# Optimization experiments

Hardware: AMD Instinct MI355X
Metric: run time of the kernel (lower is better)

## Reference

```python
import jax, jax.numpy as jnp
import numpy as np

H = 4          # number of GCN heads (hard-coded self.h = 4)
EPS = 1e-6     # MWPToolkit LayerNorm eps
B, K, D, HID = 16, 1024, 256, 256
DK = D // H


def setup_inputs() -> dict:
    key = jax.random.key(0)
    ks = jax.random.split(key, 12)
    sc = lambda fan_in: 1.0 / np.sqrt(fan_in).astype(np.float32)
    return {
        "graph_nodes": jax.random.normal(ks[0], (B, K, D), jnp.float32),
        "graph": jax.random.randint(ks[1], (B, 5, K, K), 0, 2, jnp.int32),
        # per-head GCN layer 1: GraphConvolution(indim -> hiddim)
        "Wg1": jax.random.normal(ks[2], (H, D, HID), jnp.float32) * sc(D),
        "bg1": jax.random.normal(ks[3], (H, HID), jnp.float32) * sc(D),
        # per-head GCN layer 2: GraphConvolution(hiddim -> d_k)
        "Wg2": jax.random.normal(ks[4], (H, HID, DK), jnp.float32) * sc(HID),
        "bg2": jax.random.normal(ks[5], (H, DK), jnp.float32) * sc(HID),
        # PositionwiseFeedForward: Linear(indim,hiddim) -> ReLU -> Linear(hiddim,outdim)
        "Wf1": jax.random.normal(ks[6], (D, HID), jnp.float32) * sc(D),
        "bf1": jax.random.normal(ks[7], (HID,), jnp.float32) * sc(D),
        "Wf2": jax.random.normal(ks[8], (HID, D), jnp.float32) * sc(HID),
        "bf2": jax.random.normal(ks[9], (D,), jnp.float32) * sc(HID),
        # LayerNorm(outdim) affine params
        "ln_a": jnp.ones((D,), jnp.float32),
        "ln_b": jnp.zeros((D,), jnp.float32),
    }


def reference(graph_nodes, graph, Wg1, bg1, Wg2, bg2, Wf1, bf1, Wf2, bf2, ln_a, ln_b):
    adj = graph.astype(jnp.float32)                      # (B, 5, K, K)
    # adj_list = [adj[:,1], adj[:,1], adj[:,4], adj[:,4]] -> stack heads
    adj_h = jnp.stack([adj[:, 1], adj[:, 1], adj[:, 4], adj[:, 4]])  # (H,B,K,K)

    # GCN layer 1 (all heads at once): relu(adj @ (x @ W1) + b1)
    sup1 = jnp.einsum('bkd,hdf->hbkf', graph_nodes, Wg1)            # (H,B,K,HID)
    h1 = jax.nn.relu(jnp.einsum('hbkj,hbjf->hbkf', adj_h, sup1)
                     + bg1[:, None, None, :])
    # (dropout is identity in eval)
    # GCN layer 2: adj @ (h1 @ W2) + b2
    sup2 = jnp.einsum('hbkf,hfe->hbke', h1, Wg2)                    # (H,B,K,DK)
    h2 = jnp.einsum('hbkj,hbje->hbke', adj_h, sup2) + bg2[:, None, None, :]

    # concat heads along feature dim: (B,K,H*DK) == (B,K,D)
    g = jnp.transpose(h2, (1, 2, 0, 3)).reshape(h2.shape[1], h2.shape[2], -1)

    # MWPToolkit LayerNorm: a*(x-mean)/(std+eps)+b, std unbiased (ddof=1)
    mu = g.mean(-1, keepdims=True)
    sd = jnp.std(g, axis=-1, keepdims=True, ddof=1)
    g = ln_a * (g - mu) / (sd + EPS) + ln_b + graph_nodes           # residual

    # PositionwiseFeedForward + residual (dropout identity in eval)
    ff = jax.nn.relu(g @ Wf1 + bf1) @ Wf2 + bf2
    out = ff + g
    return adj, out
```

## Files before the change

### kernel.cpp

```cpp
#include <hip/hip_runtime.h>

typedef unsigned short ushort_t;
using short8  = __attribute__((ext_vector_type(8))) short;
using floatx4 = __attribute__((ext_vector_type(4))) float;

__device__ __forceinline__ ushort_t f2bf(float f) {
  unsigned int x = __builtin_bit_cast(unsigned int, f);
  x += 0x7fffu + ((x >> 16) & 1u);
  return (ushort_t)(x >> 16);
}

__device__ __forceinline__ void gld16(const ushort_t* g, ushort_t* l) {
  __builtin_amdgcn_global_load_lds(
      (const __attribute__((address_space(1))) void*)(unsigned long long)(uintptr_t)g,
      (__attribute__((address_space(3))) void*)l, 16, 0, 0);
}

template <typename F>
__device__ __forceinline__ void gemm_tile(const ushort_t* __restrict__ A, int lda,
                                          const ushort_t* __restrict__ BT, int ldb,
                                          int K, F epi) {
  __shared__ ushort_t As[128 * 32];
  __shared__ ushort_t Bs[128 * 32];

  const int tid  = threadIdx.x;
  const int wave = tid >> 6;
  const int lane = tid & 63;
  const int l15  = lane & 15;
  const int quad = lane >> 4;
  const int wm   = wave >> 1;
  const int wn   = wave & 1;

  const int srow   = lane >> 2;
  const int schunk = (lane & 3) ^ ((lane >> 3) & 3);
  const int scol   = schunk * 8;

  const ushort_t* gA0 = A  + (size_t)(wave * 32 + srow) * lda + scol;
  const ushort_t* gA1 = gA0 + (size_t)16 * lda;
  const ushort_t* gB0 = BT + (size_t)(wave * 32 + srow) * ldb + scol;
  const ushort_t* gB1 = gB0 + (size_t)16 * ldb;
  ushort_t* lA0 = As + (wave * 32) * 32;
  ushort_t* lA1 = As + (wave * 32 + 16) * 32;
  ushort_t* lB0 = Bs + (wave * 32) * 32;
  ushort_t* lB1 = Bs + (wave * 32 + 16) * 32;

  floatx4 acc[4][4] = {};

  const int chunk_sw = quad ^ ((l15 >> 1) & 3);
  const int aoff = (wm * 64 + l15) * 32 + chunk_sw * 8;
  const int boff = (wn * 64 + l15) * 32 + chunk_sw * 8;

  for (int k0 = 0; k0 < K; k0 += 32) {
    gld16(gA0, lA0); gld16(gA1, lA1);
    gld16(gB0, lB0); gld16(gB1, lB1);
    gA0 += 32; gA1 += 32; gB0 += 32; gB1 += 32;
    __syncthreads();
    short8 af[4], bfr[4];
#pragma unroll
    for (int i = 0; i < 4; i++) af[i]  = *(const short8*)(As + aoff + i * 512);
#pragma unroll
    for (int j = 0; j < 4; j++) bfr[j] = *(const short8*)(Bs + boff + j * 512);
#pragma unroll
    for (int i = 0; i < 4; i++)
#pragma unroll
      for (int j = 0; j < 4; j++)
        acc[i][j] = __builtin_amdgcn_mfma_f32_16x16x32_bf16(af[i], bfr[j], acc[i][j], 0, 0, 0);
    __syncthreads();
  }

#pragma unroll
  for (int i = 0; i < 4; i++)
#pragma unroll
    for (int j = 0; j < 4; j++)
#pragma unroll
      for (int r = 0; r < 4; r++)
        epi(wm * 64 + i * 16 + quad * 4 + r, wn * 64 + j * 16 + l15, acc[i][j][r]);
}


__global__ __launch_bounds__(256) void k_cast(const int* __restrict__ graph,
                                              float* __restrict__ adj_out,
                                              ushort_t* __restrict__ adjb) {
  const size_t i = (size_t)blockIdx.x * 256 + threadIdx.x;
  int4 v = ((const int4*)graph)[i];
  float4 f = make_float4((float)v.x, (float)v.y, (float)v.z, (float)v.w);
  ((float4*)adj_out)[i] = f;
  const size_t e0 = i * 4;
  const unsigned sb = (unsigned)(e0 >> 20);
  const unsigned s = sb % 5u, b = sb / 5u;
  if (s == 1u || s == 4u) {
    const unsigned tt = (s == 4u) ? 1u : 0u;
    ushort4 h;
    h.x = f2bf(f.x); h.y = f2bf(f.y); h.z = f2bf(f.z); h.w = f2bf(f.w);
    *(ushort4*)(adjb + (((size_t)(b * 2 + tt)) << 20) + (e0 & 0xFFFFFu)) = h;
  }
}

__global__ __launch_bounds__(256) void k_castX(const float* __restrict__ gn,
                                               ushort_t* __restrict__ Xb) {
  const size_t i = (size_t)blockIdx.x * 256 + threadIdx.x;
  float4 f = ((const float4*)gn)[i];
  ushort4 h; h.x = f2bf(f.x); h.y = f2bf(f.y); h.z = f2bf(f.z); h.w = f2bf(f.w);
  ((ushort4*)Xb)[i] = h;
}

__global__ __launch_bounds__(256) void k_prepw(const float* __restrict__ Wg1, const float* __restrict__ Wg2,
                                               const float* __restrict__ Wf1, const float* __restrict__ Wf2,
                                               ushort_t* __restrict__ W1T, ushort_t* __restrict__ Wg2bd,
                                               ushort_t* __restrict__ Wf1T, ushort_t* __restrict__ Wf2T) {
  const int i = blockIdx.x * 256 + threadIdx.x;
  if (i < 262144) {
    const int fI = i >> 8, d = i & 255;
    const int h = fI >> 8, ff = fI & 255;
    W1T[i] = f2bf(Wg1[((h << 8) + d) * 256 + ff]);
  } else if (i < 524288) {
    const int j = i - 262144;
    const int r = j >> 10, c = j & 1023;
    const int h = r >> 6, e = r & 63;
    const float v = ((c >> 8) == h) ? Wg2[((h << 8) + (c & 255)) * 64 + e] : 0.f;
    Wg2bd[j] = f2bf(v);
  } else if (i < 589824) {
    const int j = i - 524288;
    const int n = j >> 8, k = j & 255;
    Wf1T[j] = f2bf(Wf1[k * 256 + n]);
  } else if (i < 655360) {
    const int j = i - 589824;
    const int n = j >> 8, k = j & 255;
    Wf2T[j] = f2bf(Wf2[k * 256 + n]);
  }
}


__global__ __launch_bounds__(256) void k_g1(const ushort_t* __restrict__ W1T,
                                            const ushort_t* __restrict__ Xb,
                                            ushort_t* __restrict__ sup1T) {
  const int nt = blockIdx.x, mt = blockIdx.y, b = blockIdx.z;
  const ushort_t* A  = W1T + (size_t)mt * 128 * 256;
  const ushort_t* BT = Xb + (size_t)b * 262144 + (size_t)nt * 128 * 256;
  ushort_t* C = sup1T + ((size_t)b << 20);
  gemm_tile(A, 256, BT, 256, 256, [&](int r, int c, float v) {
    C[(size_t)(mt * 128 + r) * 1024 + nt * 128 + c] = f2bf(v);
  });
}

__global__ __launch_bounds__(256) void k_g2(const ushort_t* __restrict__ adjb,
                                            const ushort_t* __restrict__ sup1T,
                                            const float* __restrict__ bg1,
                                            ushort_t* __restrict__ h1) {
  const int nt = blockIdx.x, mt = blockIdx.y, b = blockIdx.z;
  const int t = nt >> 2;
  const ushort_t* A  = adjb + ((size_t)(b * 2 + t) << 20) + (size_t)mt * 128 * 1024;
  const ushort_t* BT = sup1T + ((size_t)b << 20) + (size_t)nt * 128 * 1024;
  ushort_t* C = h1 + ((size_t)b << 20);
  const float* bias = bg1 + nt * 128;
  gemm_tile(A, 1024, BT, 1024, 1024, [&](int r, int c, float v) {
    C[(size_t)(mt * 128 + r) * 1024 + nt * 128 + c] = f2bf(fmaxf(v + bias[c], 0.f));
  });
}

__global__ __launch_bounds__(256) void k_g3(const ushort_t* __restrict__ Wg2bd,
                                            const ushort_t* __restrict__ h1,
                                            ushort_t* __restrict__ sup2T) {
  const int nt = blockIdx.x, mt = blockIdx.y, b = blockIdx.z;
  const ushort_t* A  = Wg2bd + (size_t)mt * 128 * 1024;
  const ushort_t* BT = h1 + ((size_t)b << 20) + (size_t)nt * 128 * 1024;
  ushort_t* C = sup2T + (size_t)b * 262144;
  gemm_tile(A, 1024, BT, 1024, 1024, [&](int r, int c, float v) {
    C[(size_t)(mt * 128 + r) * 1024 + nt * 128 + c] = f2bf(v);
  });
}

__global__ __launch_bounds__(256) void k_g4(const ushort_t* __restrict__ adjb,
                                            const ushort_t* __restrict__ sup2T,
                                            const float* __restrict__ bg2,
                                            float* __restrict__ g) {
  const int nt = blockIdx.x, mt = blockIdx.y, b = blockIdx.z;
  const ushort_t* A  = adjb + ((size_t)(b * 2 + nt) << 20) + (size_t)mt * 128 * 1024;
  const ushort_t* BT = sup2T + (size_t)b * 262144 + (size_t)nt * 128 * 1024;
  float* C = g + (size_t)b * 262144;
  const float* bias = bg2 + nt * 128;
  gemm_tile(A, 1024, BT, 1024, 1024, [&](int r, int c, float v) {
    C[(size_t)(mt * 128 + r) * 256 + nt * 128 + c] = v + bias[c];
  });
}

__global__ __launch_bounds__(256) void k_ln(const float* __restrict__ g, const float* __restrict__ gn,
                                            const float* __restrict__ la, const float* __restrict__ lb,
                                            float* __restrict__ glnf, ushort_t* __restrict__ glnb) {
  const int row = blockIdx.x * 4 + (threadIdx.x >> 6);
  const int lane = threadIdx.x & 63;
  const float4 x = ((const float4*)(g + (size_t)row * 256))[lane];
  float s = x.x + x.y + x.z + x.w;
#pragma unroll
  for (int o = 1; o < 64; o <<= 1) s += __shfl_xor(s, o);
  const float mu = s * (1.f / 256.f);
  const float dx = x.x - mu, dy = x.y - mu, dz = x.z - mu, dw = x.w - mu;
  float q = dx * dx + dy * dy + dz * dz + dw * dw;
#pragma unroll
  for (int o = 1; o < 64; o <<= 1) q += __shfl_xor(q, o);
  const float inv = 1.f / (sqrtf(q * (1.f / 255.f)) + 1e-6f);
  const float4 a  = ((const float4*)la)[lane];
  const float4 bb = ((const float4*)lb)[lane];
  const float4 rz = ((const float4*)(gn + (size_t)row * 256))[lane];
  float4 o;
  o.x = a.x * dx * inv + bb.x + rz.x;
  o.y = a.y * dy * inv + bb.y + rz.y;
  o.z = a.z * dz * inv + bb.z + rz.z;
  o.w = a.w * dw * inv + bb.w + rz.w;
  ((float4*)(glnf + (size_t)row * 256))[lane] = o;
  ushort4 h; h.x = f2bf(o.x); h.y = f2bf(o.y); h.z = f2bf(o.z); h.w = f2bf(o.w);
  ((ushort4*)(glnb + (size_t)row * 256))[lane] = h;
}

__global__ __launch_bounds__(256) void k_f1(const ushort_t* __restrict__ gln,
                                            const ushort_t* __restrict__ Wf1T,
                                            const float* __restrict__ bf1,
                                            ushort_t* __restrict__ tb) {
  const int nt = blockIdx.x, mt = blockIdx.y;
  const ushort_t* A  = gln + (size_t)mt * 128 * 256;
  const ushort_t* BT = Wf1T + (size_t)nt * 128 * 256;
  const float* bias = bf1 + nt * 128;
  gemm_tile(A, 256, BT, 256, 256, [&](int r, int c, float v) {
    tb[(size_t)(mt * 128 + r) * 256 + nt * 128 + c] = f2bf(fmaxf(v + bias[c], 0.f));
  });
}

__global__ __launch_bounds__(256) void k_f2(const ushort_t* __restrict__ tb,
                                            const ushort_t* __restrict__ Wf2T,
                                            const float* __restrict__ bf2,
                                            const float* __restrict__ glnf,
                                            float* __restrict__ out) {
  const int nt = blockIdx.x, mt = blockIdx.y;
  const ushort_t* A  = tb + (size_t)mt * 128 * 256;
  const ushort_t* BT = Wf2T + (size_t)nt * 128 * 256;
  const float* bias = bf2 + nt * 128;
  gemm_tile(A, 256, BT, 256, 256, [&](int r, int c, float v) {
    const size_t idx = (size_t)(mt * 128 + r) * 256 + nt * 128 + c;
    out[idx] = v + bias[c] + glnf[idx];
  });
}

extern "C" void kernel_launch(void* const* d_in, const int* in_sizes, int n_in,
                              void* d_out, int out_size, void* d_ws, size_t ws_size,
                              hipStream_t stream) {
  const float* gnodes = (const float*)d_in[0];
  const int*   graph  = (const int*)d_in[1];
  const float* Wg1 = (const float*)d_in[2];
  const float* bg1 = (const float*)d_in[3];
  const float* Wg2 = (const float*)d_in[4];
  const float* bg2 = (const float*)d_in[5];
  const float* Wf1 = (const float*)d_in[6];
  const float* bf1 = (const float*)d_in[7];
  const float* Wf2 = (const float*)d_in[8];
  const float* bf2 = (const float*)d_in[9];
  const float* ln_a = (const float*)d_in[10];
  const float* ln_b = (const float*)d_in[11];

  float* adj_out = (float*)d_out;
  float* out     = (float*)d_out + 83886080;

  char* ws = (char*)d_ws;
  ushort_t* adjb  = (ushort_t*)(ws);
  ushort_t* Xb    = (ushort_t*)(ws + 67108864);
  ushort_t* W1T   = (ushort_t*)(ws + 75497472);
  ushort_t* Wg2bd = (ushort_t*)(ws + 76021760);
  ushort_t* Wf1T  = (ushort_t*)(ws + 76546048);
  ushort_t* Wf2T  = (ushort_t*)(ws + 76677120);
  ushort_t* sup1T = (ushort_t*)(ws + 76808192);
  ushort_t* h1    = (ushort_t*)(ws + 110362624);
  ushort_t* sup2T = (ushort_t*)(ws + 143917056);
  float*    gbuf  = (float*)(ws + 76808192);
  float*    glnf  = (float*)(ws + 76808192 + 16777216);
  ushort_t* glnb  = (ushort_t*)(ws + 110362624);
  ushort_t* tbuf  = (ushort_t*)(ws + 110362624 + 8388608);

  k_cast <<<81920, 256, 0, stream>>>(graph, adj_out, adjb);
  k_castX<<<4096, 256, 0, stream>>>(gnodes, Xb);
  k_prepw<<<2560, 256, 0, stream>>>(Wg1, Wg2, Wf1, Wf2, W1T, Wg2bd, Wf1T, Wf2T);

  k_g1<<<dim3(8, 8, 16), 256, 0, stream>>>(W1T, Xb, sup1T);
  k_g2<<<dim3(8, 8, 16), 256, 0, stream>>>(adjb, sup1T, bg1, h1);
  k_g3<<<dim3(8, 2, 16), 256, 0, stream>>>(Wg2bd, h1, sup2T);
  k_g4<<<dim3(2, 8, 16), 256, 0, stream>>>(adjb, sup2T, bg2, gbuf);

  k_ln<<<4096, 256, 0, stream>>>(gbuf, gnodes, ln_a, ln_b, glnf, glnb);

  k_f1<<<dim3(2, 128), 256, 0, stream>>>(glnb, Wf1T, bf1, tbuf);
  k_f2<<<dim3(2, 128), 256, 0, stream>>>(tbuf, Wf2T, bf2, glnf, out);
}
```

Baseline: 736.4 us.

## Reassociate first GCN layer as (adj@X)@W1 and deepen GEMM K-tile to 64

Layer 1 now computes adj@X once per adjacency type (two per batch), then multiplies by the per-head W1. The previous code did adj@(X@W1) across all four heads with an inner dimension of 1024, so this cuts the large adjacency GEMM work roughly in half. It adds a transposed bf16 copy of X and splits the adjacency cast so the f32 adj output is written by its own kernel at the end. The shared GEMM tile also loads 64 K-elements per stage with a new swizzle, halving the number of barriers per tile. This uses more LDS per block, and the extra bf16 rounding of AX changes numerics slightly.

```diff
diff --git a/kernel.cpp b/kernel.cpp
--- a/kernel.cpp
+++ b/kernel.cpp
@@ -20,8 +20,8 @@
 __device__ __forceinline__ void gemm_tile(const ushort_t* __restrict__ A, int lda,
                                           const ushort_t* __restrict__ BT, int ldb,
                                           int K, F epi) {
-  __shared__ ushort_t As[128 * 32];
-  __shared__ ushort_t Bs[128 * 32];
+  __shared__ ushort_t As[128 * 64];
+  __shared__ ushort_t Bs[128 * 64];
 
   const int tid  = threadIdx.x;
   const int wave = tid >> 6;
@@ -31,40 +31,43 @@
   const int wm   = wave >> 1;
   const int wn   = wave & 1;
 
-  const int srow   = lane >> 2;
-  const int schunk = (lane & 3) ^ ((lane >> 3) & 3);
-  const int scol   = schunk * 8;
-
-  const ushort_t* gA0 = A  + (size_t)(wave * 32 + srow) * lda + scol;
-  const ushort_t* gA1 = gA0 + (size_t)16 * lda;
-  const ushort_t* gB0 = BT + (size_t)(wave * 32 + srow) * ldb + scol;
-  const ushort_t* gB1 = gB0 + (size_t)16 * ldb;
-  ushort_t* lA0 = As + (wave * 32) * 32;
-  ushort_t* lA1 = As + (wave * 32 + 16) * 32;
-  ushort_t* lB0 = Bs + (wave * 32) * 32;
-  ushort_t* lB1 = Bs + (wave * 32 + 16) * 32;
+  const int srow8  = lane >> 3;
+  const int schunk = lane & 7;
+  const int gcol   = ((schunk ^ srow8) * 8);
+
+  const ushort_t* gA = A  + (size_t)(wave * 32 + srow8) * lda + gcol;
+  const ushort_t* gB = BT + (size_t)(wave * 32 + srow8) * ldb + gcol;
+  ushort_t* lA = As + (wave * 32) * 64;
+  ushort_t* lB = Bs + (wave * 32) * 64;
 
   floatx4 acc[4][4] = {};
 
-  const int chunk_sw = quad ^ ((l15 >> 1) & 3);
-  const int aoff = (wm * 64 + l15) * 32 + chunk_sw * 8;
-  const int boff = (wn * 64 + l15) * 32 + chunk_sw * 8;
-
-  for (int k0 = 0; k0 < K; k0 += 32) {
-    gld16(gA0, lA0); gld16(gA1, lA1);
-    gld16(gB0, lB0); gld16(gB1, lB1);
-    gA0 += 32; gA1 += 32; gB0 += 32; gB1 += 32;
+  const int arow0 = (wm * 64 + l15) * 64;
+  const int brow0 = (wn * 64 + l15) * 64;
+  const int cx    = l15 & 7;
+
+  for (int k0 = 0; k0 < K; k0 += 64) {
+#pragma unroll
+    for (int ci = 0; ci < 4; ci++) {
+      gld16(gA + (size_t)(ci * 8) * lda, lA + ci * 512);
+      gld16(gB + (size_t)(ci * 8) * ldb, lB + ci * 512);
+    }
+    gA += 64; gB += 64;
     __syncthreads();
-    short8 af[4], bfr[4];
-#pragma unroll
-    for (int i = 0; i < 4; i++) af[i]  = *(const short8*)(As + aoff + i * 512);
-#pragma unroll
-    for (int j = 0; j < 4; j++) bfr[j] = *(const short8*)(Bs + boff + j * 512);
-#pragma unroll
-    for (int i = 0; i < 4; i++)
-#pragma unroll
-      for (int j = 0; j < 4; j++)
-        acc[i][j] = __builtin_amdgcn_mfma_f32_16x16x32_bf16(af[i], bfr[j], acc[i][j], 0, 0, 0);
+#pragma unroll
+    for (int ks = 0; ks < 2; ks++) {
+      const int cs = ((ks * 4 + quad) ^ cx) * 8;
+      short8 af[4], bfr[4];
+#pragma unroll
+      for (int i = 0; i < 4; i++) af[i]  = *(const short8*)(As + arow0 + i * 1024 + cs);
+#pragma unroll
+      for (int j = 0; j < 4; j++) bfr[j] = *(const short8*)(Bs + brow0 + j * 1024 + cs);
+#pragma unroll
+      for (int i = 0; i < 4; i++)
+#pragma unroll
+        for (int j = 0; j < 4; j++)
+          acc[i][j] = __builtin_amdgcn_mfma_f32_16x16x32_bf16(af[i], bfr[j], acc[i][j], 0, 0, 0);
+    }
     __syncthreads();
   }
 
@@ -78,30 +81,48 @@
 }
 
 
-__global__ __launch_bounds__(256) void k_cast(const int* __restrict__ graph,
-                                              float* __restrict__ adj_out,
+__global__ __launch_bounds__(256) void k_adjb(const int* __restrict__ graph,
                                               ushort_t* __restrict__ adjb) {
   const size_t i = (size_t)blockIdx.x * 256 + threadIdx.x;
+  const size_t e0 = i * 4;
+  const unsigned bt = (unsigned)(e0 >> 20);
+  const unsigned b = bt >> 1, t = bt & 1;
+  const unsigned s = t ? 4u : 1u;
+  int4 v = *(const int4*)(graph + (((size_t)(b * 5 + s)) << 20) + (e0 & 0xFFFFFu));
+  ushort4 h;
+  h.x = f2bf((float)v.x); h.y = f2bf((float)v.y);
+  h.z = f2bf((float)v.z); h.w = f2bf((float)v.w);
+  *(ushort4*)(adjb + e0) = h;
+}
+
+__global__ __launch_bounds__(256) void k_adjf32(const int* __restrict__ graph,
+                                                float* __restrict__ adj_out) {
+  const size_t i = (size_t)blockIdx.x * 256 + threadIdx.x;
   int4 v = ((const int4*)graph)[i];
-  float4 f = make_float4((float)v.x, (float)v.y, (float)v.z, (float)v.w);
-  ((float4*)adj_out)[i] = f;
-  const size_t e0 = i * 4;
-  const unsigned sb = (unsigned)(e0 >> 20);
-  const unsigned s = sb % 5u, b = sb / 5u;
-  if (s == 1u || s == 4u) {
-    const unsigned tt = (s == 4u) ? 1u : 0u;
+  ((float4*)adj_out)[i] = make_float4((float)v.x, (float)v.y, (float)v.z, (float)v.w);
+}
+
+__global__ __launch_bounds__(256) void k_xt(const float* __restrict__ gn,
+                                            ushort_t* __restrict__ XT) {
+  __shared__ float t[64][68];
+  const int b = blockIdx.z, dt = blockIdx.y, kt = blockIdx.x;
+  const int r  = threadIdx.x >> 4;
+  const int c4 = (threadIdx.x & 15) * 4;
+#pragma unroll
+  for (int rr = 0; rr < 4; rr++) {
+    const int kl = rr * 16 + r;
+    float4 v = *(const float4*)(gn + ((size_t)(b * 1024 + kt * 64 + kl)) * 256 + dt * 64 + c4);
+    t[kl][c4] = v.x; t[kl][c4 + 1] = v.y; t[kl][c4 + 2] = v.z; t[kl][c4 + 3] = v.w;
+  }
+  __syncthreads();
+#pragma unroll
+  for (int rr = 0; rr < 4; rr++) {
+    const int dl = rr * 16 + r;
     ushort4 h;
-    h.x = f2bf(f.x); h.y = f2bf(f.y); h.z = f2bf(f.z); h.w = f2bf(f.w);
-    *(ushort4*)(adjb + (((size_t)(b * 2 + tt)) << 20) + (e0 & 0xFFFFFu)) = h;
+    h.x = f2bf(t[c4][dl]);     h.y = f2bf(t[c4 + 1][dl]);
+    h.z = f2bf(t[c4 + 2][dl]); h.w = f2bf(t[c4 + 3][dl]);
+    *(ushort4*)(XT + ((size_t)(b * 256 + dt * 64 + dl)) * 1024 + kt * 64 + c4) = h;
   }
-}
-
-__global__ __launch_bounds__(256) void k_castX(const float* __restrict__ gn,
-                                               ushort_t* __restrict__ Xb) {
-  const size_t i = (size_t)blockIdx.x * 256 + threadIdx.x;
-  float4 f = ((const float4*)gn)[i];
-  ushort4 h; h.x = f2bf(f.x); h.y = f2bf(f.y); h.z = f2bf(f.z); h.w = f2bf(f.w);
-  ((ushort4*)Xb)[i] = h;
 }
 
 __global__ __launch_bounds__(256) void k_prepw(const float* __restrict__ Wg1, const float* __restrict__ Wg2,
@@ -131,29 +152,30 @@
 }
 
 
-__global__ __launch_bounds__(256) void k_g1(const ushort_t* __restrict__ W1T,
-                                            const ushort_t* __restrict__ Xb,
-                                            ushort_t* __restrict__ sup1T) {
-  const int nt = blockIdx.x, mt = blockIdx.y, b = blockIdx.z;
-  const ushort_t* A  = W1T + (size_t)mt * 128 * 256;
-  const ushort_t* BT = Xb + (size_t)b * 262144 + (size_t)nt * 128 * 256;
-  ushort_t* C = sup1T + ((size_t)b << 20);
-  gemm_tile(A, 256, BT, 256, 256, [&](int r, int c, float v) {
-    C[(size_t)(mt * 128 + r) * 1024 + nt * 128 + c] = f2bf(v);
-  });
-}
-
-__global__ __launch_bounds__(256) void k_g2(const ushort_t* __restrict__ adjb,
-                                            const ushort_t* __restrict__ sup1T,
+__global__ __launch_bounds__(256) void k_ax(const ushort_t* __restrict__ adjb,
+                                            const ushort_t* __restrict__ XT,
+                                            ushort_t* __restrict__ AX) {
+  const int nt = blockIdx.x, mt = blockIdx.y, bt = blockIdx.z;
+  const int b = bt >> 1;
+  const ushort_t* A  = adjb + ((size_t)bt << 20) + (size_t)mt * 128 * 1024;
+  const ushort_t* BT = XT + ((size_t)b << 18) + (size_t)nt * 128 * 1024;
+  ushort_t* C = AX + ((size_t)bt << 18);
+  gemm_tile(A, 1024, BT, 1024, 1024, [&](int r, int c, float v) {
+    C[(size_t)(mt * 128 + r) * 256 + nt * 128 + c] = f2bf(v);
+  });
+}
+
+__global__ __launch_bounds__(256) void k_h1(const ushort_t* __restrict__ AX,
+                                            const ushort_t* __restrict__ W1T,
                                             const float* __restrict__ bg1,
                                             ushort_t* __restrict__ h1) {
   const int nt = blockIdx.x, mt = blockIdx.y, b = blockIdx.z;
   const int t = nt >> 2;
-  const ushort_t* A  = adjb + ((size_t)(b * 2 + t) << 20) + (size_t)mt * 128 * 1024;
-  const ushort_t* BT = sup1T + ((size_t)b << 20) + (size_t)nt * 128 * 1024;
+  const ushort_t* A  = AX + ((size_t)(b * 2 + t) << 18) + (size_t)mt * 128 * 256;
+  const ushort_t* BT = W1T + (size_t)nt * 128 * 256;
   ushort_t* C = h1 + ((size_t)b << 20);
   const float* bias = bg1 + nt * 128;
-  gemm_tile(A, 1024, BT, 1024, 1024, [&](int r, int c, float v) {
+  gemm_tile(A, 256, BT, 256, 256, [&](int r, int c, float v) {
     C[(size_t)(mt * 128 + r) * 1024 + nt * 128 + c] = f2bf(fmaxf(v + bias[c], 0.f));
   });
 }
@@ -261,25 +283,25 @@
 
   char* ws = (char*)d_ws;
   ushort_t* adjb  = (ushort_t*)(ws);
-  ushort_t* Xb    = (ushort_t*)(ws + 67108864);
+  ushort_t* XT    = (ushort_t*)(ws + 67108864);
   ushort_t* W1T   = (ushort_t*)(ws + 75497472);
   ushort_t* Wg2bd = (ushort_t*)(ws + 76021760);
   ushort_t* Wf1T  = (ushort_t*)(ws + 76546048);
   ushort_t* Wf2T  = (ushort_t*)(ws + 76677120);
-  ushort_t* sup1T = (ushort_t*)(ws + 76808192);
-  ushort_t* h1    = (ushort_t*)(ws + 110362624);
-  ushort_t* sup2T = (ushort_t*)(ws + 143917056);
-  float*    gbuf  = (float*)(ws + 76808192);
-  float*    glnf  = (float*)(ws + 76808192 + 16777216);
-  ushort_t* glnb  = (ushort_t*)(ws + 110362624);
-  ushort_t* tbuf  = (ushort_t*)(ws + 110362624 + 8388608);
-
-  k_cast <<<81920, 256, 0, stream>>>(graph, adj_out, adjb);
-  k_castX<<<4096, 256, 0, stream>>>(gnodes, Xb);
+  ushort_t* AX    = (ushort_t*)(ws + 76808192);
+  ushort_t* h1    = (ushort_t*)(ws + 93585408);
+  ushort_t* sup2T = (ushort_t*)(ws + 127139840);
+  float*    gbuf  = (float*)(ws + 135528448);
+  float*    glnf  = (float*)(ws + 152305664);
+  ushort_t* glnb  = (ushort_t*)(ws + 169082880);
+  ushort_t* tbuf  = (ushort_t*)(ws + 177471488);
+
+  k_adjb <<<32768, 256, 0, stream>>>(graph, adjb);
+  k_xt   <<<dim3(16, 4, 16), 256, 0, stream>>>(gnodes, XT);
   k_prepw<<<2560, 256, 0, stream>>>(Wg1, Wg2, Wf1, Wf2, W1T, Wg2bd, Wf1T, Wf2T);
 
-  k_g1<<<dim3(8, 8, 16), 256, 0, stream>>>(W1T, Xb, sup1T);
-  k_g2<<<dim3(8, 8, 16), 256, 0, stream>>>(adjb, sup1T, bg1, h1);
+  k_ax<<<dim3(2, 8, 32), 256, 0, stream>>>(adjb, XT, AX);
+  k_h1<<<dim3(8, 8, 16), 256, 0, stream>>>(AX, W1T, bg1, h1);
   k_g3<<<dim3(8, 2, 16), 256, 0, stream>>>(Wg2bd, h1, sup2T);
   k_g4<<<dim3(2, 8, 16), 256, 0, stream>>>(adjb, sup2T, bg2, gbuf);
 
@@ -287,4 +309,6 @@
 
   k_f1<<<dim3(2, 128), 256, 0, stream>>>(glnb, Wf1T, bf1, tbuf);
   k_f2<<<dim3(2, 128), 256, 0, stream>>>(tbuf, Wf2T, bf2, glnf, out);
-}
+
+  k_adjf32<<<81920, 256, 0, stream>>>(graph, adj_out);
+}
```

Measured after the change: 720.8 us. 2.1% less time.
